# Performance work log

Hardware: AMD Instinct MI355X
Metric: run time of the kernel (lower is better)

## Reference

```python
import jax, jax.numpy as jnp
import numpy as np
from jax import lax

L = 64          # filter_length
C = 64          # n_channels
B = 64          # batch
T = 4096        # time steps per call


def _sliding_max(a, k):
    # a: [B, C, T + k - 1] -> [B, C, T], windowed max, stride 1, VALID
    return lax.reduce_window(a, -jnp.inf, lax.max, (1, 1, k), (1, 1, 1), 'VALID')


def setup_inputs() -> dict:
    key = jax.random.key(0)
    x = jax.random.normal(key, (B, C, T), dtype=jnp.float32)
    # State buffers as lazily allocated by the module on first forward:
    prev_input = jnp.full((B, C, L - 1), -jnp.inf, dtype=jnp.float32)
    prev_max_out = jnp.full((B, C, L - 1), jnp.inf, dtype=jnp.float32)
    return {'x': x, 'prev_input': prev_input, 'prev_max_out': prev_max_out}


def reference(x, prev_input, prev_max_out):
    # max-pool over [prev_input, x] with kernel L, stride 1 (causal streaming max)
    max_input = jnp.concatenate([prev_input, x], axis=-1)        # [B, C, T+L-1]
    max_out = _sliding_max(max_input, L)                         # [B, C, T]
    # min-pool over [prev_max_out, max_out] via negated max-pool
    min_input = jnp.concatenate([prev_max_out, max_out], axis=-1)  # [B, C, T+L-1]
    out = -_sliding_max(-min_input, L)                           # [B, C, T]
    return out
```

## Files before the change

### kernel.cpp

```cpp
#include <hip/hip_runtime.h>
#include <math.h>


#define TT   4096
#define LF   64
#define PADN (LF - 1)
#define PLEN (TT + PADN)

#define DPP_UPD(v, ctrl, rmask) \
  __int_as_float(__builtin_amdgcn_update_dpp(__float_as_int(v), __float_as_int(v), ctrl, rmask, 0xF, false))

#define SCAN_MAX(p) do { \
  p = fmaxf(p, DPP_UPD(p, 0x111, 0xF)); \
  p = fmaxf(p, DPP_UPD(p, 0x112, 0xF)); \
  p = fmaxf(p, DPP_UPD(p, 0x114, 0xF)); \
  p = fmaxf(p, DPP_UPD(p, 0x118, 0xF)); \
  p = fmaxf(p, DPP_UPD(p, 0x142, 0xA)); \
  p = fmaxf(p, DPP_UPD(p, 0x143, 0xC)); \
} while (0)

#define SCAN_MIN(p) do { \
  p = fminf(p, DPP_UPD(p, 0x111, 0xF)); \
  p = fminf(p, DPP_UPD(p, 0x112, 0xF)); \
  p = fminf(p, DPP_UPD(p, 0x114, 0xF)); \
  p = fminf(p, DPP_UPD(p, 0x118, 0xF)); \
  p = fminf(p, DPP_UPD(p, 0x142, 0xA)); \
  p = fminf(p, DPP_UPD(p, 0x143, 0xC)); \
} while (0)

__global__ __launch_bounds__(512)
void mmh_kernel(const float* __restrict__ x,
                const float* __restrict__ prev_input,
                const float* __restrict__ prev_max_out,
                float* __restrict__ out)
{
    __shared__ float s_in[PLEN + 2];
    __shared__ float s_mid[PLEN + 2];

    const int row  = blockIdx.x;
    const int tid  = threadIdx.x;
    const int lane = tid & 63;
    const int wave = tid >> 6;

    const float* xrow  = x            + (size_t)row * TT;
    const float* pirow = prev_input   + (size_t)row * PADN;
    const float* pmrow = prev_max_out + (size_t)row * PADN;
    float*       orow  = out          + (size_t)row * TT;

    const int rev4 = (63 - lane) << 2;

    for (int i = tid; i < TT / 4; i += blockDim.x) {
        float4 v = reinterpret_cast<const float4*>(xrow)[i];
        *reinterpret_cast<float4*>(&s_in[64 + 4 * i]) = v;
    }
    if (tid < PADN) {
        s_in[1 + tid]  = pirow[tid];
        s_mid[1 + tid] = pmrow[tid];
    }
    __syncthreads();

    #pragma unroll
    for (int cc = 0; cc < 8; ++cc) {
        const int base = wave * 512 + cc * 64;
        float a0r = s_in[1 + base + 63 - lane];
        float a1e = s_in[base + 64 + lane];
        if (lane == 0) a1e = -INFINITY;
        SCAN_MAX(a0r);
        SCAN_MAX(a1e);
        float sfx = __int_as_float(
            __builtin_amdgcn_ds_bpermute(rev4, __float_as_int(a0r)));
        s_mid[64 + base + lane] = fmaxf(sfx, a1e);
    }
    __syncthreads();

    #pragma unroll
    for (int cc = 0; cc < 8; ++cc) {
        const int base = wave * 512 + cc * 64;
        float a0r = s_mid[1 + base + 63 - lane];
        float a1e = s_mid[base + 64 + lane];
        if (lane == 0) a1e = INFINITY;
        SCAN_MIN(a0r);
        SCAN_MIN(a1e);
        float sfx = __int_as_float(
            __builtin_amdgcn_ds_bpermute(rev4, __float_as_int(a0r)));
        orow[base + lane] = fminf(sfx, a1e);
    }
}

extern "C" void kernel_launch(void* const* d_in, const int* in_sizes, int n_in,
                              void* d_out, int out_size, void* d_ws, size_t ws_size,
                              hipStream_t stream) {
    const float* x            = (const float*)d_in[0];
    const float* prev_input   = (const float*)d_in[1];
    const float* prev_max_out = (const float*)d_in[2];
    float*       out          = (float*)d_out;

    mmh_kernel<<<64 * 64, 512, 0, stream>>>(x, prev_input, prev_max_out, out);
}
```

Measured before the change: 130.1 us.

## Process four elements per lane with row-level DPP scans instead of full-wave scans

Reworks the sliding max/min so that each lane handles four consecutive elements with float4 LDS loads. Each lane does an in-register prefix/suffix over its four values, then combines across 16-lane rows with DPP row shifts, which drops the cross-row DPP steps and the ds_bpermute reversal. The input is stored into LDS shifted by one element so the chunks stay 16-byte aligned, and the output is written as float4. This cuts per-element shuffle and LDS-instruction counts, at the cost of more intricate boundary handling (misaligned staging loads, edge fixups) that could hide correctness bugs.

```diff
diff --git a/kernel.cpp b/kernel.cpp
--- a/kernel.cpp
+++ b/kernel.cpp
@@ -3,30 +3,57 @@
 
 
 #define TT   4096
-#define LF   64
-#define PADN (LF - 1)
-#define PLEN (TT + PADN)
+#define PADN 63
+#define SLEN 4160
 
-#define DPP_UPD(v, ctrl, rmask) \
-  __int_as_float(__builtin_amdgcn_update_dpp(__float_as_int(v), __float_as_int(v), ctrl, rmask, 0xF, false))
+template<int CTRL>
+__device__ __forceinline__ float dpp_self(float v) {
+  return __int_as_float(__builtin_amdgcn_update_dpp(
+      __float_as_int(v), __float_as_int(v), CTRL, 0xF, 0xF, false));
+}
+template<int CTRL>
+__device__ __forceinline__ float dpp_old(float oldv, float v) {
+  return __int_as_float(__builtin_amdgcn_update_dpp(
+      __float_as_int(oldv), __float_as_int(v), CTRL, 0xF, 0xF, false));
+}
 
-#define SCAN_MAX(p) do { \
-  p = fmaxf(p, DPP_UPD(p, 0x111, 0xF)); \
-  p = fmaxf(p, DPP_UPD(p, 0x112, 0xF)); \
-  p = fmaxf(p, DPP_UPD(p, 0x114, 0xF)); \
-  p = fmaxf(p, DPP_UPD(p, 0x118, 0xF)); \
-  p = fmaxf(p, DPP_UPD(p, 0x142, 0xA)); \
-  p = fmaxf(p, DPP_UPD(p, 0x143, 0xC)); \
-} while (0)
+template<bool IS_MAX>
+__device__ __forceinline__ void chunk_windows(const float* sbuf, int b, int lane,
+                                              float r[4], float& u_out) {
+  const float ID = IS_MAX ? -INFINITY : INFINITY;
+#define OPF(x, y) (IS_MAX ? fmaxf((x), (y)) : fminf((x), (y)))
+  const float4 a0 = *reinterpret_cast<const float4*>(sbuf + b + 4 * lane);
+  const float4 a1 = *reinterpret_cast<const float4*>(sbuf + b + 64 + 4 * lane);
 
-#define SCAN_MIN(p) do { \
-  p = fminf(p, DPP_UPD(p, 0x111, 0xF)); \
-  p = fminf(p, DPP_UPD(p, 0x112, 0xF)); \
-  p = fminf(p, DPP_UPD(p, 0x114, 0xF)); \
-  p = fminf(p, DPP_UPD(p, 0x118, 0xF)); \
-  p = fminf(p, DPP_UPD(p, 0x142, 0xA)); \
-  p = fminf(p, DPP_UPD(p, 0x143, 0xC)); \
-} while (0)
+  float s3 = a0.w;
+  float s2 = OPF(a0.z, s3);
+  float s1 = OPF(a0.y, s2);
+  float s0 = OPF(a0.x, s1);
+  float t = s0;
+  t = OPF(t, dpp_self<0x101>(t));
+  t = OPF(t, dpp_self<0x102>(t));
+  t = OPF(t, dpp_self<0x104>(t));
+  t = OPF(t, dpp_self<0x108>(t));
+  float E = dpp_old<0x101>(ID, t);
+
+  float p0 = a1.x;
+  float p1 = OPF(p0, a1.y);
+  float p2 = OPF(p1, a1.z);
+  float p3 = OPF(p2, a1.w);
+  float u = p3;
+  u = OPF(u, dpp_self<0x111>(u));
+  u = OPF(u, dpp_self<0x112>(u));
+  u = OPF(u, dpp_self<0x114>(u));
+  u = OPF(u, dpp_self<0x118>(u));
+  float Ep = dpp_old<0x111>(ID, u);
+
+  r[0] = OPF(OPF(s0, E), Ep);
+  r[1] = OPF(OPF(s1, E), OPF(Ep, p0));
+  r[2] = OPF(OPF(s2, E), OPF(Ep, p1));
+  r[3] = OPF(OPF(s3, E), OPF(Ep, p2));
+  u_out = u;
+#undef OPF
+}
 
 __global__ __launch_bounds__(512)
 void mmh_kernel(const float* __restrict__ x,
@@ -34,8 +61,8 @@
                 const float* __restrict__ prev_max_out,
                 float* __restrict__ out)
 {
-    __shared__ float s_in[PLEN + 2];
-    __shared__ float s_mid[PLEN + 2];
+    __shared__ float s_in[SLEN];
+    __shared__ float s_mid[SLEN];
 
     const int row  = blockIdx.x;
     const int tid  = threadIdx.x;
@@ -47,43 +74,38 @@
     const float* pmrow = prev_max_out + (size_t)row * PADN;
     float*       orow  = out          + (size_t)row * TT;
 
-    const int rev4 = (63 - lane) << 2;
+    for (int i = tid; i < 1023; i += 512) {
+        float4 v = *reinterpret_cast<const float4*>(xrow + 4 * i);
+        float  e = xrow[4 * i + 4];
+        float4 w = make_float4(v.y, v.z, v.w, e);
+        *reinterpret_cast<float4*>(&s_in[64 + 4 * i]) = w;
+    }
+    if (tid < 63)       { s_in[tid] = pirow[tid]; s_mid[tid] = pmrow[tid]; }
+    else if (tid == 63) { s_in[63] = xrow[0]; }
+    else if (tid < 67)  { s_in[4156 + tid - 64] = xrow[4093 + tid - 64]; }
+    else if (tid == 67) { s_in[4159] = -INFINITY; }
+    else if (tid == 68) { s_mid[4159] = INFINITY; }
+    __syncthreads();
 
-    for (int i = tid; i < TT / 4; i += blockDim.x) {
-        float4 v = reinterpret_cast<const float4*>(xrow)[i];
-        *reinterpret_cast<float4*>(&s_in[64 + 4 * i]) = v;
-    }
-    if (tid < PADN) {
-        s_in[1 + tid]  = pirow[tid];
-        s_mid[1 + tid] = pmrow[tid];
+    #pragma unroll
+    for (int cc = 0; cc < 2; ++cc) {
+        const int b = (wave + 8 * cc) << 8;
+        float r[4], u;
+        chunk_windows<true>(s_in, b, lane, r, u);
+        float  w3 = dpp_old<0x101>(u, r[0]);
+        float4 wv = make_float4(r[1], r[2], r[3], w3);
+        *reinterpret_cast<float4*>(&s_mid[64 + b + 4 * lane]) = wv;
+        if ((b | lane) == 0) s_mid[63] = r[0];
     }
     __syncthreads();
 
     #pragma unroll
-    for (int cc = 0; cc < 8; ++cc) {
-        const int base = wave * 512 + cc * 64;
-        float a0r = s_in[1 + base + 63 - lane];
-        float a1e = s_in[base + 64 + lane];
-        if (lane == 0) a1e = -INFINITY;
-        SCAN_MAX(a0r);
-        SCAN_MAX(a1e);
-        float sfx = __int_as_float(
-            __builtin_amdgcn_ds_bpermute(rev4, __float_as_int(a0r)));
-        s_mid[64 + base + lane] = fmaxf(sfx, a1e);
-    }
-    __syncthreads();
-
-    #pragma unroll
-    for (int cc = 0; cc < 8; ++cc) {
-        const int base = wave * 512 + cc * 64;
-        float a0r = s_mid[1 + base + 63 - lane];
-        float a1e = s_mid[base + 64 + lane];
-        if (lane == 0) a1e = INFINITY;
-        SCAN_MIN(a0r);
-        SCAN_MIN(a1e);
-        float sfx = __int_as_float(
-            __builtin_amdgcn_ds_bpermute(rev4, __float_as_int(a0r)));
-        orow[base + lane] = fminf(sfx, a1e);
+    for (int cc = 0; cc < 2; ++cc) {
+        const int b = (wave + 8 * cc) << 8;
+        float r[4], u;
+        chunk_windows<false>(s_mid, b, lane, r, u);
+        *reinterpret_cast<float4*>(orow + b + 4 * lane) =
+            make_float4(r[0], r[1], r[2], r[3]);
     }
 }
 
```

Measured after the change: 116.5 us. 10.4% less time.
